# Kernel tuning notes

Measured on AMD Instinct MI355X. Metric: run time of the kernel, lower is better.

The kernel has to match this reference:

```python
import jax, jax.numpy as jnp
import numpy as np

silu = jax.nn.silu
B, L, H, IN = 128, 2048, 8, 37
NL = 8  # 4 encoder + 4 decoder SE3 layers, stacked


def _se3_layer(h, pos, eW1, eb1, eW2, eb2, pW1, pb1, pW2, nW1, nb1, nW2, nb2):
    # chain graph: row = 0..N-2, col = 1..N-1 (as in the torch arange edges)
    rel = pos[1:] - pos[:-1]                      # [N-1, 3]
    dist = jnp.linalg.norm(rel, axis=-1, keepdims=True)
    ef = jnp.concatenate([h[:-1], h[1:], dist], axis=-1)   # [N-1, 2H+1]
    ea = silu(ef @ eW1 + eb1) @ eW2 + eb2                   # edge_mlp
    dp = silu(ea @ pW1 + pb1) @ pW2                         # pos_mlp (no bias on last)
    pos_upd = jnp.zeros_like(pos).at[:-1].add(dp).at[1:].add(-dp)
    node_upd = jnp.zeros_like(h).at[:-1].add(ea).at[1:].add(ea)
    h_out = silu(jnp.concatenate([h, node_upd], axis=-1) @ nW1 + nb1) @ nW2 + nb2
    return h_out, pos + 0.1 * pos_upd


def setup_inputs() -> dict:
    key = jax.random.key(0)
    ks = jax.random.split(key, 64)
    i = iter(range(64))
    def p(shape, s=0.1):
        return (jax.random.normal(ks[next(i)], shape, jnp.float32) * s)
    inp = {
        "atom_positions": jax.random.normal(ks[next(i)], (B, L, IN, 3), jnp.float32),
        "atom_mask": (jax.random.uniform(ks[next(i)], (B, L, IN)) < 0.8).astype(jnp.float32),
        "emb_W": p((IN, H)), "emb_b": p((H,)),
        "posemb_W1": p((3, H)), "posemb_b1": p((H,)),
        "posemb_W2": p((H, H)), "posemb_b2": p((H,)),
        # stacked SE3 conv params: layers 0-3 encoder, 4-7 decoder
        "conv_eW1": p((NL, 2 * H + 1, H)), "conv_eb1": p((NL, H)),
        "conv_eW2": p((NL, H, H)), "conv_eb2": p((NL, H)),
        "conv_pW1": p((NL, H, H)), "conv_pb1": p((NL, H)),
        "conv_pW2": p((NL, H, 3)),
        "conv_nW1": p((NL, 2 * H, H)), "conv_nb1": p((NL, H)),
        "conv_nW2": p((NL, H, H)), "conv_nb2": p((NL, H)),
        "tol_W1": p((H, H)), "tol_b1": p((H,)),
        "tol_W2": p((H, H)), "tol_b2": p((H,)),
        "froml_W1": p((H, H)), "froml_b1": p((H,)),
        "froml_W2": p((H, H)), "froml_b2": p((H,)),
        "posdec_W1": p((H, 2 * H)), "posdec_b1": p((2 * H,)),
        "posdec_W2": p((2 * H, IN * 3)), "posdec_b2": p((IN * 3,)),
        "maskdec_W": p((H, IN)), "maskdec_b": p((IN,)),
    }
    return inp


def reference(atom_positions, atom_mask, emb_W, emb_b, posemb_W1, posemb_b1,
              posemb_W2, posemb_b2, conv_eW1, conv_eb1, conv_eW2, conv_eb2,
              conv_pW1, conv_pb1, conv_pW2, conv_nW1, conv_nb1, conv_nW2,
              conv_nb2, tol_W1, tol_b1, tol_W2, tol_b2, froml_W1, froml_b1,
              froml_W2, froml_b2, posdec_W1, posdec_b1, posdec_W2, posdec_b2,
              maskdec_W, maskdec_b):
    # ---- encode ----
    h = atom_mask @ emb_W + emb_b                              # [B,L,H]
    m = atom_mask[..., None]
    mean_pos = (atom_positions * m).sum(axis=2) / (m.sum(axis=2) + 1e-8)  # [B,L,3]
    pos_feat = silu(mean_pos @ posemb_W1 + posemb_b1) @ posemb_W2 + posemb_b2
    h = (h + pos_feat).reshape(B * L, H)
    pos = mean_pos.reshape(B * L, 3)
    for li in range(4):
        h, pos = _se3_layer(h, pos, conv_eW1[li], conv_eb1[li], conv_eW2[li],
                            conv_eb2[li], conv_pW1[li], conv_pb1[li], conv_pW2[li],
                            conv_nW1[li], conv_nb1[li], conv_nW2[li], conv_nb2[li])
    h = h.reshape(B, L, H)
    z = silu(h @ tol_W1 + tol_b1) @ tol_W2 + tol_b2            # [B,L,latent]
    # ---- decode ----
    h = silu(z @ froml_W1 + froml_b1) @ froml_W2 + froml_b2
    h = h.reshape(B * L, H)
    pos = pos  # already flat [B*L, 3]
    for li in range(4, 8):
        h, pos = _se3_layer(h, pos, conv_eW1[li], conv_eb1[li], conv_eW2[li],
                            conv_eb2[li], conv_pW1[li], conv_pb1[li], conv_pW2[li],
                            conv_nW1[li], conv_nb1[li], conv_nW2[li], conv_nb2[li])
    h = h.reshape(B, L, H)
    pos_out = (silu(h @ posdec_W1 + posdec_b1) @ posdec_W2 + posdec_b2)
    pos_out = pos_out.reshape(B, L, IN, 3)
    mask_out = h @ maskdec_W + maskdec_b                       # [B,L,IN]
    return pos_out, mask_out
```

## Files before the change

### kernel.cpp

```cpp
#include <hip/hip_runtime.h>

#define NTOT 262144
#define NLAY 8
#define TOUT 240

__device__ __forceinline__ float silu_f(float x) {
    return x * (1.0f / (1.0f + __expf(-x)));
}

__global__ __launch_bounds__(256) void k_encode(
    const float* __restrict__ ap, const float* __restrict__ amask,
    const float* __restrict__ embW, const float* __restrict__ embB,
    const float* __restrict__ peW1, const float* __restrict__ peB1,
    const float* __restrict__ peW2, const float* __restrict__ peB2,
    float* __restrict__ h0, float* __restrict__ pos0)
{
    __shared__ alignas(16) float sM[64 * 37];
    __shared__ alignas(16) float sA[64 * 111];
    __shared__ alignas(16) float sW[37 * 8];
    const int tid = threadIdx.x;
    const long nb = (long)blockIdx.x * 64;

    if (tid < 74) ((float4*)sW)[tid] = ((const float4*)embW)[tid];
    const float4* gm = (const float4*)(amask + nb * 37);
    float4* sm4 = (float4*)sM;
    #pragma unroll 1
    for (int i = tid; i < 64 * 37 / 4; i += 256) sm4[i] = gm[i];
    const float4* ga = (const float4*)(ap + nb * 111);
    float4* sa4 = (float4*)sA;
    #pragma unroll 1
    for (int i = tid; i < 64 * 111 / 4; i += 256) sa4[i] = ga[i];
    __syncthreads();

    const int n = tid >> 2;
    const int p = tid & 3;
    const int k0 = p * 10;
    const int k1 = (p == 3) ? 37 : k0 + 10;

    const float* mrow = sM + n * 37;
    const float* arow = sA + n * 111;
    float hacc[8] = {0, 0, 0, 0, 0, 0, 0, 0};
    float ps0 = 0.f, ps1 = 0.f, ps2 = 0.f, msum = 0.f;
    #pragma unroll 1
    for (int k = k0; k < k1; ++k) {
        float mv = mrow[k];
        msum += mv;
        const float4* wr = (const float4*)(sW + k * 8);
        float4 w0 = wr[0], w1 = wr[1];
        hacc[0] += mv * w0.x; hacc[1] += mv * w0.y;
        hacc[2] += mv * w0.z; hacc[3] += mv * w0.w;
        hacc[4] += mv * w1.x; hacc[5] += mv * w1.y;
        hacc[6] += mv * w1.z; hacc[7] += mv * w1.w;
        ps0 += mv * arow[k * 3 + 0];
        ps1 += mv * arow[k * 3 + 1];
        ps2 += mv * arow[k * 3 + 2];
    }
    #pragma unroll
    for (int m = 1; m <= 2; m <<= 1) {
        msum += __shfl_xor(msum, m);
        ps0 += __shfl_xor(ps0, m);
        ps1 += __shfl_xor(ps1, m);
        ps2 += __shfl_xor(ps2, m);
        #pragma unroll
        for (int j = 0; j < 8; ++j) hacc[j] += __shfl_xor(hacc[j], m);
    }

    float inv = 1.0f / (msum + 1e-8f);
    float mp0 = ps0 * inv, mp1 = ps1 * inv, mp2 = ps2 * inv;
    float q[8];
    #pragma unroll
    for (int j = 0; j < 8; ++j) {
        float a = peB1[j];
        a += mp0 * peW1[0 * 8 + j];
        a += mp1 * peW1[1 * 8 + j];
        a += mp2 * peW1[2 * 8 + j];
        q[j] = silu_f(a);
    }
    #pragma unroll
    for (int j = 0; j < 8; ++j) {
        float a = peB2[j] + embB[j];
        #pragma unroll
        for (int r = 0; r < 8; ++r) a += q[r] * peW2[r * 8 + j];
        hacc[j] += a;
    }
    const long g = nb + n;
    if (p == 0) ((float4*)(h0 + g * 8))[0] = make_float4(hacc[0], hacc[1], hacc[2], hacc[3]);
    if (p == 1) ((float4*)(h0 + g * 8))[1] = make_float4(hacc[4], hacc[5], hacc[6], hacc[7]);
    if (p == 2) ((float4*)pos0)[g] = make_float4(mp0, mp1, mp2, 0.f);
}

__global__ __launch_bounds__(256) void k_stack(
    const float* __restrict__ h0, const float* __restrict__ pos0,
    float* __restrict__ hfin,
    const float* __restrict__ ceW1, const float* __restrict__ ceB1,
    const float* __restrict__ ceW2, const float* __restrict__ ceB2,
    const float* __restrict__ cpW1, const float* __restrict__ cpB1,
    const float* __restrict__ cpW2,
    const float* __restrict__ cnW1, const float* __restrict__ cnB1,
    const float* __restrict__ cnW2, const float* __restrict__ cnB2,
    const float* __restrict__ tW1, const float* __restrict__ tB1,
    const float* __restrict__ tW2, const float* __restrict__ tB2,
    const float* __restrict__ fW1, const float* __restrict__ fB1,
    const float* __restrict__ fW2, const float* __restrict__ fB2)
{
    __shared__ float4 sH[512];
    __shared__ float4 sP[256];
    __shared__ float4 sE[512];
    __shared__ float4 sD[256];
    const int t = threadIdx.x;
    const int g0 = blockIdx.x * TOUT;
    const int g = g0 - 8 + t;

    float4 z4 = make_float4(0.f, 0.f, 0.f, 0.f);
    float4 ha = z4, hb = z4, pa = z4;
    if (g >= 0 && g < NTOT) {
        const float4* hp = (const float4*)(h0 + (long)g * 8);
        ha = hp[0];
        hb = hp[1];
        pa = ((const float4*)pos0)[g];
    }
    sH[t * 2] = ha;
    sH[t * 2 + 1] = hb;
    sP[t] = pa;
    __syncthreads();

    const int tp = (t < 255) ? (t + 1) : t;
    const int tm = (t > 0) ? (t - 1) : t;
    float hn[8] = {0, 0, 0, 0, 0, 0, 0, 0};

    #pragma unroll 1
    for (int li = 0; li < NLAY; ++li) {
        float hl[8], hr[8];
        {
            float4 a = sH[t * 2], b = sH[t * 2 + 1];
            hl[0] = a.x; hl[1] = a.y; hl[2] = a.z; hl[3] = a.w;
            hl[4] = b.x; hl[5] = b.y; hl[6] = b.z; hl[7] = b.w;
            float4 c = sH[tp * 2], d = sH[tp * 2 + 1];
            hr[0] = c.x; hr[1] = c.y; hr[2] = c.z; hr[3] = c.w;
            hr[4] = d.x; hr[5] = d.y; hr[6] = d.z; hr[7] = d.w;
        }
        float4 plv = sP[t], prv = sP[tp];
        float r0 = prv.x - plv.x, r1 = prv.y - plv.y, r2 = prv.z - plv.z;
        float dist = sqrtf(r0 * r0 + r1 * r1 + r2 * r2);

        const float* wE1 = ceW1 + li * 136;
        const float* bE1 = ceB1 + li * 8;
        const float* wE2 = ceW2 + li * 64;
        const float* bE2 = ceB2 + li * 8;
        const float* wP1 = cpW1 + li * 64;
        const float* bP1 = cpB1 + li * 8;
        const float* wP2 = cpW2 + li * 24;
        const float* wN1 = cnW1 + li * 128;
        const float* bN1 = cnB1 + li * 8;
        const float* wN2 = cnW2 + li * 64;
        const float* bN2 = cnB2 + li * 8;

        float t1[8];
        #pragma unroll
        for (int j = 0; j < 8; ++j) {
            float a = bE1[j];
            #pragma unroll
            for (int r = 0; r < 8; ++r) a += hl[r] * wE1[r * 8 + j];
            #pragma unroll
            for (int r = 0; r < 8; ++r) a += hr[r] * wE1[64 + r * 8 + j];
            a += dist * wE1[128 + j];
            t1[j] = silu_f(a);
        }
        float ea[8];
        #pragma unroll
        for (int j = 0; j < 8; ++j) {
            float a = bE2[j];
            #pragma unroll
            for (int r = 0; r < 8; ++r) a += t1[r] * wE2[r * 8 + j];
            ea[j] = a;
        }
        float q[8];
        #pragma unroll
        for (int j = 0; j < 8; ++j) {
            float a = bP1[j];
            #pragma unroll
            for (int r = 0; r < 8; ++r) a += ea[r] * wP1[r * 8 + j];
            q[j] = silu_f(a);
        }
        float dp0 = 0.f, dp1 = 0.f, dp2 = 0.f;
        #pragma unroll
        for (int r = 0; r < 8; ++r) {
            dp0 += q[r] * wP2[r * 3 + 0];
            dp1 += q[r] * wP2[r * 3 + 1];
            dp2 += q[r] * wP2[r * 3 + 2];
        }
        sE[t * 2] = make_float4(ea[0], ea[1], ea[2], ea[3]);
        sE[t * 2 + 1] = make_float4(ea[4], ea[5], ea[6], ea[7]);
        sD[t] = make_float4(dp0, dp1, dp2, 0.f);
        __syncthreads();

        float nu[8] = {0, 0, 0, 0, 0, 0, 0, 0};
        float pu0 = 0.f, pu1 = 0.f, pu2 = 0.f;
        if (g < NTOT - 1) {
            #pragma unroll
            for (int j = 0; j < 8; ++j) nu[j] += ea[j];
            pu0 += dp0; pu1 += dp1; pu2 += dp2;
        }
        if (g > 0) {
            float4 a = sE[tm * 2], b = sE[tm * 2 + 1];
            nu[0] += a.x; nu[1] += a.y; nu[2] += a.z; nu[3] += a.w;
            nu[4] += b.x; nu[5] += b.y; nu[6] += b.z; nu[7] += b.w;
            float4 dl = sD[tm];
            pu0 -= dl.x; pu1 -= dl.y; pu2 -= dl.z;
        }
        float u[8];
        #pragma unroll
        for (int j = 0; j < 8; ++j) {
            float a = bN1[j];
            #pragma unroll
            for (int r = 0; r < 8; ++r) a += hl[r] * wN1[r * 8 + j];
            #pragma unroll
            for (int r = 0; r < 8; ++r) a += nu[r] * wN1[64 + r * 8 + j];
            u[j] = silu_f(a);
        }
        #pragma unroll
        for (int j = 0; j < 8; ++j) {
            float a = bN2[j];
            #pragma unroll
            for (int r = 0; r < 8; ++r) a += u[r] * wN2[r * 8 + j];
            hn[j] = a;
        }
        float pn0 = plv.x + 0.1f * pu0;
        float pn1 = plv.y + 0.1f * pu1;
        float pn2 = plv.z + 0.1f * pu2;

        if (li == 3) {
            float a8[8];
            #pragma unroll
            for (int j = 0; j < 8; ++j) {
                float a = tB1[j];
                #pragma unroll
                for (int r = 0; r < 8; ++r) a += hn[r] * tW1[r * 8 + j];
                a8[j] = silu_f(a);
            }
            float zz[8];
            #pragma unroll
            for (int j = 0; j < 8; ++j) {
                float a = tB2[j];
                #pragma unroll
                for (int r = 0; r < 8; ++r) a += a8[r] * tW2[r * 8 + j];
                zz[j] = a;
            }
            float b8[8];
            #pragma unroll
            for (int j = 0; j < 8; ++j) {
                float a = fB1[j];
                #pragma unroll
                for (int r = 0; r < 8; ++r) a += zz[r] * fW1[r * 8 + j];
                b8[j] = silu_f(a);
            }
            #pragma unroll
            for (int j = 0; j < 8; ++j) {
                float a = fB2[j];
                #pragma unroll
                for (int r = 0; r < 8; ++r) a += b8[r] * fW2[r * 8 + j];
                hn[j] = a;
            }
        }

        const int winLo2 = max(0, g0 - 7 + li);
        const int winHi2 = min(NTOT, g0 + 247 - li);
        if (g >= winLo2 && g < winHi2) {
            sH[t * 2] = make_float4(hn[0], hn[1], hn[2], hn[3]);
            sH[t * 2 + 1] = make_float4(hn[4], hn[5], hn[6], hn[7]);
            sP[t] = make_float4(pn0, pn1, pn2, 0.f);
        }
        __syncthreads();
    }

    if (t >= 8 && t < 8 + TOUT && g < NTOT) {
        float4* hd = (float4*)(hfin + (long)g * 8);
        hd[0] = make_float4(hn[0], hn[1], hn[2], hn[3]);
        hd[1] = make_float4(hn[4], hn[5], hn[6], hn[7]);
    }
}

__global__ __launch_bounds__(256) void k_decode(
    const float* __restrict__ hfin,
    const float* __restrict__ dW1, const float* __restrict__ dB1,
    const float* __restrict__ dW2, const float* __restrict__ dB2,
    const float* __restrict__ mW, const float* __restrict__ mB,
    float* __restrict__ out)
{
    __shared__ alignas(16) float sh[128 * 8];
    __shared__ alignas(16) float st1[128 * 16];
    const int tid = threadIdx.x;
    const long nb = (long)blockIdx.x * 128;

    ((float4*)sh)[tid] = ((const float4*)(hfin + nb * 8))[tid];
    __syncthreads();

    {
        const int n = tid >> 1;
        const int c0 = (tid & 1) * 8;
        const float4* h4 = (const float4*)(sh + n * 8);
        float4 h0v = h4[0], h1v = h4[1];
        float hr[8] = {h0v.x, h0v.y, h0v.z, h0v.w, h1v.x, h1v.y, h1v.z, h1v.w};
        #pragma unroll
        for (int jj = 0; jj < 8; ++jj) {
            int j = c0 + jj;
            float a = dB1[j];
            #pragma unroll
            for (int r = 0; r < 8; ++r) a += hr[r] * dW1[r * 16 + j];
            st1[n * 16 + j] = silu_f(a);
        }
    }
    __syncthreads();

    if (tid < 222) {
        const int half = (tid >= 111) ? 1 : 0;
        const int j = tid - half * 111;
        float w[16];
        #pragma unroll
        for (int r = 0; r < 16; ++r) w[r] = dW2[r * 111 + j];
        const float bj = dB2[j];
        float* op = out + nb * 111 + j;
        #pragma unroll 2
        for (int n = half; n < 128; n += 2) {
            const float4* t4 = (const float4*)(st1 + n * 16);
            float4 a0 = t4[0], a1 = t4[1], a2 = t4[2], a3 = t4[3];
            float acc = bj;
            acc += a0.x * w[0] + a0.y * w[1] + a0.z * w[2] + a0.w * w[3];
            acc += a1.x * w[4] + a1.y * w[5] + a1.z * w[6] + a1.w * w[7];
            acc += a2.x * w[8] + a2.y * w[9] + a2.z * w[10] + a2.w * w[11];
            acc += a3.x * w[12] + a3.y * w[13] + a3.z * w[14] + a3.w * w[15];
            op[n * 111] = acc;
        }
        const int g6 = tid / 37;
        const int j2 = tid - g6 * 37;
        float wm[8];
        #pragma unroll
        for (int r = 0; r < 8; ++r) wm[r] = mW[r * 37 + j2];
        const float bm = mB[j2];
        float* omp_ = out + (long)NTOT * 111 + nb * 37 + j2;
        #pragma unroll 1
        for (int n = g6; n < 128; n += 6) {
            const float4* h4 = (const float4*)(sh + n * 8);
            float4 h0v = h4[0], h1v = h4[1];
            float acc = bm;
            acc += h0v.x * wm[0] + h0v.y * wm[1] + h0v.z * wm[2] + h0v.w * wm[3];
            acc += h1v.x * wm[4] + h1v.y * wm[5] + h1v.z * wm[6] + h1v.w * wm[7];
            omp_[n * 37] = acc;
        }
    }
}

extern "C" void kernel_launch(void* const* d_in, const int* in_sizes, int n_in,
                              void* d_out, int out_size, void* d_ws, size_t ws_size,
                              hipStream_t stream) {
    const float* ap     = (const float*)d_in[0];
    const float* amask  = (const float*)d_in[1];
    const float* embW   = (const float*)d_in[2];
    const float* embB   = (const float*)d_in[3];
    const float* peW1   = (const float*)d_in[4];
    const float* peB1   = (const float*)d_in[5];
    const float* peW2   = (const float*)d_in[6];
    const float* peB2   = (const float*)d_in[7];
    const float* ceW1   = (const float*)d_in[8];
    const float* ceB1   = (const float*)d_in[9];
    const float* ceW2   = (const float*)d_in[10];
    const float* ceB2   = (const float*)d_in[11];
    const float* cpW1   = (const float*)d_in[12];
    const float* cpB1   = (const float*)d_in[13];
    const float* cpW2   = (const float*)d_in[14];
    const float* cnW1   = (const float*)d_in[15];
    const float* cnB1   = (const float*)d_in[16];
    const float* cnW2   = (const float*)d_in[17];
    const float* cnB2   = (const float*)d_in[18];
    const float* tW1    = (const float*)d_in[19];
    const float* tB1    = (const float*)d_in[20];
    const float* tW2    = (const float*)d_in[21];
    const float* tB2    = (const float*)d_in[22];
    const float* fW1    = (const float*)d_in[23];
    const float* fB1    = (const float*)d_in[24];
    const float* fW2    = (const float*)d_in[25];
    const float* fB2    = (const float*)d_in[26];
    const float* dW1    = (const float*)d_in[27];
    const float* dB1    = (const float*)d_in[28];
    const float* dW2    = (const float*)d_in[29];
    const float* dB2    = (const float*)d_in[30];
    const float* mW     = (const float*)d_in[31];
    const float* mB     = (const float*)d_in[32];

    float* h0   = (float*)d_ws;
    float* pos0 = h0 + (size_t)NTOT * 8;
    float* hfin = pos0 + (size_t)NTOT * 4;
    float* out  = (float*)d_out;

    k_encode<<<NTOT / 64, 256, 0, stream>>>(ap, amask, embW, embB,
                                            peW1, peB1, peW2, peB2, h0, pos0);
    k_stack<<<(NTOT + TOUT - 1) / TOUT, 256, 0, stream>>>(
        h0, pos0, hfin,
        ceW1, ceB1, ceW2, ceB2, cpW1, cpB1, cpW2,
        cnW1, cnB1, cnW2, cnB2,
        tW1, tB1, tW2, tB2, fW1, fB1, fW2, fB2);
    k_decode<<<NTOT / 128, 256, 0, stream>>>(hfin, dW1, dB1, dW2, dB2, mW, mB, out);
}
```

Baseline: 435.0 us.

## Run SE3 layer stack per wavefront with shuffles instead of shared-memory barriers

The layer-stack kernel now assigns each 64-lane wavefront its own chain segment, with two nodes per lane. Neighbour features and edge messages are exchanged with lane shuffles instead of shared memory and block-wide barriers. This removes all LDS traffic and __syncthreads from the eight-layer loop. The cost is a larger relative halo (16 of 128 nodes recomputed versus 16 of 256). It also swaps divisions and sqrt for the hardware approximate rcp/sqrt builtins, which may change precision slightly.

```diff
diff --git a/kernel.cpp b/kernel.cpp
--- a/kernel.cpp
+++ b/kernel.cpp
@@ -2,10 +2,11 @@
 
 #define NTOT 262144
 #define NLAY 8
-#define TOUT 240
+#define SEGOUT 112
+#define NSEG ((NTOT + SEGOUT - 1) / SEGOUT)
 
 __device__ __forceinline__ float silu_f(float x) {
-    return x * (1.0f / (1.0f + __expf(-x)));
+    return x * __builtin_amdgcn_rcpf(1.0f + __expf(-x));
 }
 
 __global__ __launch_bounds__(256) void k_encode(
@@ -65,7 +66,7 @@
         for (int j = 0; j < 8; ++j) hacc[j] += __shfl_xor(hacc[j], m);
     }
 
-    float inv = 1.0f / (msum + 1e-8f);
+    float inv = __builtin_amdgcn_rcpf(msum + 1e-8f);
     float mp0 = ps0 * inv, mp1 = ps1 * inv, mp2 = ps2 * inv;
     float q[8];
     #pragma unroll
@@ -87,6 +88,115 @@
     if (p == 0) ((float4*)(h0 + g * 8))[0] = make_float4(hacc[0], hacc[1], hacc[2], hacc[3]);
     if (p == 1) ((float4*)(h0 + g * 8))[1] = make_float4(hacc[4], hacc[5], hacc[6], hacc[7]);
     if (p == 2) ((float4*)pos0)[g] = make_float4(mp0, mp1, mp2, 0.f);
+}
+
+
+__device__ __forceinline__ void edge_mlp(
+    const float* __restrict__ wE1, const float* __restrict__ bE1,
+    const float* __restrict__ wE2, const float* __restrict__ bE2,
+    const float* __restrict__ wP1, const float* __restrict__ bP1,
+    const float* __restrict__ wP2,
+    const float* hl, const float* hr, float r0, float r1, float r2,
+    float* ea, float& dp0, float& dp1, float& dp2)
+{
+    float dist = __builtin_amdgcn_sqrtf(r0 * r0 + r1 * r1 + r2 * r2);
+    float t1[8];
+    #pragma unroll
+    for (int j = 0; j < 8; ++j) {
+        float a = bE1[j];
+        #pragma unroll
+        for (int r = 0; r < 8; ++r) a += hl[r] * wE1[r * 8 + j];
+        #pragma unroll
+        for (int r = 0; r < 8; ++r) a += hr[r] * wE1[64 + r * 8 + j];
+        a += dist * wE1[128 + j];
+        t1[j] = silu_f(a);
+    }
+    #pragma unroll
+    for (int j = 0; j < 8; ++j) {
+        float a = bE2[j];
+        #pragma unroll
+        for (int r = 0; r < 8; ++r) a += t1[r] * wE2[r * 8 + j];
+        ea[j] = a;
+    }
+    float q[8];
+    #pragma unroll
+    for (int j = 0; j < 8; ++j) {
+        float a = bP1[j];
+        #pragma unroll
+        for (int r = 0; r < 8; ++r) a += ea[r] * wP1[r * 8 + j];
+        q[j] = silu_f(a);
+    }
+    dp0 = 0.f; dp1 = 0.f; dp2 = 0.f;
+    #pragma unroll
+    for (int r = 0; r < 8; ++r) {
+        dp0 += q[r] * wP2[r * 3 + 0];
+        dp1 += q[r] * wP2[r * 3 + 1];
+        dp2 += q[r] * wP2[r * 3 + 2];
+    }
+}
+
+__device__ __forceinline__ void node_mlp(
+    const float* __restrict__ wN1, const float* __restrict__ bN1,
+    const float* __restrict__ wN2, const float* __restrict__ bN2,
+    const float* hl, const float* nu, float* hn)
+{
+    float u[8];
+    #pragma unroll
+    for (int j = 0; j < 8; ++j) {
+        float a = bN1[j];
+        #pragma unroll
+        for (int r = 0; r < 8; ++r) a += hl[r] * wN1[r * 8 + j];
+        #pragma unroll
+        for (int r = 0; r < 8; ++r) a += nu[r] * wN1[64 + r * 8 + j];
+        u[j] = silu_f(a);
+    }
+    #pragma unroll
+    for (int j = 0; j < 8; ++j) {
+        float a = bN2[j];
+        #pragma unroll
+        for (int r = 0; r < 8; ++r) a += u[r] * wN2[r * 8 + j];
+        hn[j] = a;
+    }
+}
+
+__device__ __forceinline__ void latent_mlp(
+    const float* __restrict__ tW1, const float* __restrict__ tB1,
+    const float* __restrict__ tW2, const float* __restrict__ tB2,
+    const float* __restrict__ fW1, const float* __restrict__ fB1,
+    const float* __restrict__ fW2, const float* __restrict__ fB2,
+    float* hn)
+{
+    float a8[8];
+    #pragma unroll
+    for (int j = 0; j < 8; ++j) {
+        float a = tB1[j];
+        #pragma unroll
+        for (int r = 0; r < 8; ++r) a += hn[r] * tW1[r * 8 + j];
+        a8[j] = silu_f(a);
+    }
+    float zz[8];
+    #pragma unroll
+    for (int j = 0; j < 8; ++j) {
+        float a = tB2[j];
+        #pragma unroll
+        for (int r = 0; r < 8; ++r) a += a8[r] * tW2[r * 8 + j];
+        zz[j] = a;
+    }
+    float b8[8];
+    #pragma unroll
+    for (int j = 0; j < 8; ++j) {
+        float a = fB1[j];
+        #pragma unroll
+        for (int r = 0; r < 8; ++r) a += zz[r] * fW1[r * 8 + j];
+        b8[j] = silu_f(a);
+    }
+    #pragma unroll
+    for (int j = 0; j < 8; ++j) {
+        float a = fB2[j];
+        #pragma unroll
+        for (int r = 0; r < 8; ++r) a += b8[r] * fW2[r * 8 + j];
+        hn[j] = a;
+    }
 }
 
 __global__ __launch_bounds__(256) void k_stack(
@@ -103,46 +213,39 @@
     const float* __restrict__ fW1, const float* __restrict__ fB1,
     const float* __restrict__ fW2, const float* __restrict__ fB2)
 {
-    __shared__ float4 sH[512];
-    __shared__ float4 sP[256];
-    __shared__ float4 sE[512];
-    __shared__ float4 sD[256];
-    const int t = threadIdx.x;
-    const int g0 = blockIdx.x * TOUT;
-    const int g = g0 - 8 + t;
-
-    float4 z4 = make_float4(0.f, 0.f, 0.f, 0.f);
-    float4 ha = z4, hb = z4, pa = z4;
-    if (g >= 0 && g < NTOT) {
-        const float4* hp = (const float4*)(h0 + (long)g * 8);
-        ha = hp[0];
-        hb = hp[1];
-        pa = ((const float4*)pos0)[g];
-    }
-    sH[t * 2] = ha;
-    sH[t * 2 + 1] = hb;
-    sP[t] = pa;
-    __syncthreads();
-
-    const int tp = (t < 255) ? (t + 1) : t;
-    const int tm = (t > 0) ? (t - 1) : t;
-    float hn[8] = {0, 0, 0, 0, 0, 0, 0, 0};
+    const int lane = threadIdx.x & 63;
+    const int seg  = blockIdx.x * 4 + (threadIdx.x >> 6);
+    const int base = seg * SEGOUT - 8;
+    const int nA   = base + 2 * lane;
+    const int nB   = nA + 1;
+
+    float hA[8] = {0, 0, 0, 0, 0, 0, 0, 0};
+    float hB[8] = {0, 0, 0, 0, 0, 0, 0, 0};
+    float pA0 = 0.f, pA1 = 0.f, pA2 = 0.f;
+    float pB0 = 0.f, pB1 = 0.f, pB2 = 0.f;
+    if (nA >= 0 && nA < NTOT) {
+        const float4* hp = (const float4*)(h0 + (long)nA * 8);
+        float4 a = hp[0], b = hp[1];
+        hA[0] = a.x; hA[1] = a.y; hA[2] = a.z; hA[3] = a.w;
+        hA[4] = b.x; hA[5] = b.y; hA[6] = b.z; hA[7] = b.w;
+        float4 p = ((const float4*)pos0)[nA];
+        pA0 = p.x; pA1 = p.y; pA2 = p.z;
+    }
+    if (nB >= 0 && nB < NTOT) {
+        const float4* hp = (const float4*)(h0 + (long)nB * 8);
+        float4 a = hp[0], b = hp[1];
+        hB[0] = a.x; hB[1] = a.y; hB[2] = a.z; hB[3] = a.w;
+        hB[4] = b.x; hB[5] = b.y; hB[6] = b.z; hB[7] = b.w;
+        float4 p = ((const float4*)pos0)[nB];
+        pB0 = p.x; pB1 = p.y; pB2 = p.z;
+    }
+
+    const bool eA = (nA >= 0) && (nB < NTOT);
+    const bool eB = (nB >= 0) && (nB + 1 < NTOT);
+    const bool eL = (nA >= 1) && (nA < NTOT);
 
     #pragma unroll 1
     for (int li = 0; li < NLAY; ++li) {
-        float hl[8], hr[8];
-        {
-            float4 a = sH[t * 2], b = sH[t * 2 + 1];
-            hl[0] = a.x; hl[1] = a.y; hl[2] = a.z; hl[3] = a.w;
-            hl[4] = b.x; hl[5] = b.y; hl[6] = b.z; hl[7] = b.w;
-            float4 c = sH[tp * 2], d = sH[tp * 2 + 1];
-            hr[0] = c.x; hr[1] = c.y; hr[2] = c.z; hr[3] = c.w;
-            hr[4] = d.x; hr[5] = d.y; hr[6] = d.z; hr[7] = d.w;
-        }
-        float4 plv = sP[t], prv = sP[tp];
-        float r0 = prv.x - plv.x, r1 = prv.y - plv.y, r2 = prv.z - plv.z;
-        float dist = sqrtf(r0 * r0 + r1 * r1 + r2 * r2);
-
         const float* wE1 = ceW1 + li * 136;
         const float* bE1 = ceB1 + li * 8;
         const float* wE2 = ceW2 + li * 64;
@@ -155,128 +258,67 @@
         const float* wN2 = cnW2 + li * 64;
         const float* bN2 = cnB2 + li * 8;
 
-        float t1[8];
+        float hc[8], pc0, pc1, pc2;
+        #pragma unroll
+        for (int j = 0; j < 8; ++j) hc[j] = __shfl_down(hA[j], 1);
+        pc0 = __shfl_down(pA0, 1);
+        pc1 = __shfl_down(pA1, 1);
+        pc2 = __shfl_down(pA2, 1);
+
+        float eaA[8], dpA0, dpA1, dpA2;
+        edge_mlp(wE1, bE1, wE2, bE2, wP1, bP1, wP2,
+                 hA, hB, pB0 - pA0, pB1 - pA1, pB2 - pA2, eaA, dpA0, dpA1, dpA2);
+        float eaB[8], dpB0, dpB1, dpB2;
+        edge_mlp(wE1, bE1, wE2, bE2, wP1, bP1, wP2,
+                 hB, hc, pc0 - pB0, pc1 - pB1, pc2 - pB2, eaB, dpB0, dpB1, dpB2);
+
+        float eaL[8], dpL0, dpL1, dpL2;
+        #pragma unroll
+        for (int j = 0; j < 8; ++j) eaL[j] = __shfl_up(eaB[j], 1);
+        dpL0 = __shfl_up(dpB0, 1);
+        dpL1 = __shfl_up(dpB1, 1);
+        dpL2 = __shfl_up(dpB2, 1);
+
+        float nuA[8], nuB[8];
         #pragma unroll
         for (int j = 0; j < 8; ++j) {
-            float a = bE1[j];
-            #pragma unroll
-            for (int r = 0; r < 8; ++r) a += hl[r] * wE1[r * 8 + j];
-            #pragma unroll
-            for (int r = 0; r < 8; ++r) a += hr[r] * wE1[64 + r * 8 + j];
-            a += dist * wE1[128 + j];
-            t1[j] = silu_f(a);
-        }
-        float ea[8];
-        #pragma unroll
-        for (int j = 0; j < 8; ++j) {
-            float a = bE2[j];
-            #pragma unroll
-            for (int r = 0; r < 8; ++r) a += t1[r] * wE2[r * 8 + j];
-            ea[j] = a;
-        }
-        float q[8];
-        #pragma unroll
-        for (int j = 0; j < 8; ++j) {
-            float a = bP1[j];
-            #pragma unroll
-            for (int r = 0; r < 8; ++r) a += ea[r] * wP1[r * 8 + j];
-            q[j] = silu_f(a);
-        }
-        float dp0 = 0.f, dp1 = 0.f, dp2 = 0.f;
-        #pragma unroll
-        for (int r = 0; r < 8; ++r) {
-            dp0 += q[r] * wP2[r * 3 + 0];
-            dp1 += q[r] * wP2[r * 3 + 1];
-            dp2 += q[r] * wP2[r * 3 + 2];
-        }
-        sE[t * 2] = make_float4(ea[0], ea[1], ea[2], ea[3]);
-        sE[t * 2 + 1] = make_float4(ea[4], ea[5], ea[6], ea[7]);
-        sD[t] = make_float4(dp0, dp1, dp2, 0.f);
-        __syncthreads();
-
-        float nu[8] = {0, 0, 0, 0, 0, 0, 0, 0};
-        float pu0 = 0.f, pu1 = 0.f, pu2 = 0.f;
-        if (g < NTOT - 1) {
-            #pragma unroll
-            for (int j = 0; j < 8; ++j) nu[j] += ea[j];
-            pu0 += dp0; pu1 += dp1; pu2 += dp2;
-        }
-        if (g > 0) {
-            float4 a = sE[tm * 2], b = sE[tm * 2 + 1];
-            nu[0] += a.x; nu[1] += a.y; nu[2] += a.z; nu[3] += a.w;
-            nu[4] += b.x; nu[5] += b.y; nu[6] += b.z; nu[7] += b.w;
-            float4 dl = sD[tm];
-            pu0 -= dl.x; pu1 -= dl.y; pu2 -= dl.z;
-        }
-        float u[8];
-        #pragma unroll
-        for (int j = 0; j < 8; ++j) {
-            float a = bN1[j];
-            #pragma unroll
-            for (int r = 0; r < 8; ++r) a += hl[r] * wN1[r * 8 + j];
-            #pragma unroll
-            for (int r = 0; r < 8; ++r) a += nu[r] * wN1[64 + r * 8 + j];
-            u[j] = silu_f(a);
-        }
-        #pragma unroll
-        for (int j = 0; j < 8; ++j) {
-            float a = bN2[j];
-            #pragma unroll
-            for (int r = 0; r < 8; ++r) a += u[r] * wN2[r * 8 + j];
-            hn[j] = a;
-        }
-        float pn0 = plv.x + 0.1f * pu0;
-        float pn1 = plv.y + 0.1f * pu1;
-        float pn2 = plv.z + 0.1f * pu2;
+            nuA[j] = (eA ? eaA[j] : 0.f) + (eL ? eaL[j] : 0.f);
+            nuB[j] = (eB ? eaB[j] : 0.f) + (eA ? eaA[j] : 0.f);
+        }
+        float puA0 = (eA ? dpA0 : 0.f) - (eL ? dpL0 : 0.f);
+        float puA1 = (eA ? dpA1 : 0.f) - (eL ? dpL1 : 0.f);
+        float puA2 = (eA ? dpA2 : 0.f) - (eL ? dpL2 : 0.f);
+        float puB0 = (eB ? dpB0 : 0.f) - (eA ? dpA0 : 0.f);
+        float puB1 = (eB ? dpB1 : 0.f) - (eA ? dpA1 : 0.f);
+        float puB2 = (eB ? dpB2 : 0.f) - (eA ? dpA2 : 0.f);
+
+        float hnA[8], hnB[8];
+        node_mlp(wN1, bN1, wN2, bN2, hA, nuA, hnA);
+        node_mlp(wN1, bN1, wN2, bN2, hB, nuB, hnB);
+
+        pA0 += 0.1f * puA0; pA1 += 0.1f * puA1; pA2 += 0.1f * puA2;
+        pB0 += 0.1f * puB0; pB1 += 0.1f * puB1; pB2 += 0.1f * puB2;
 
         if (li == 3) {
-            float a8[8];
-            #pragma unroll
-            for (int j = 0; j < 8; ++j) {
-                float a = tB1[j];
-                #pragma unroll
-                for (int r = 0; r < 8; ++r) a += hn[r] * tW1[r * 8 + j];
-                a8[j] = silu_f(a);
-            }
-            float zz[8];
-            #pragma unroll
-            for (int j = 0; j < 8; ++j) {
-                float a = tB2[j];
-                #pragma unroll
-                for (int r = 0; r < 8; ++r) a += a8[r] * tW2[r * 8 + j];
-                zz[j] = a;
-            }
-            float b8[8];
-            #pragma unroll
-            for (int j = 0; j < 8; ++j) {
-                float a = fB1[j];
-                #pragma unroll
-                for (int r = 0; r < 8; ++r) a += zz[r] * fW1[r * 8 + j];
-                b8[j] = silu_f(a);
-            }
-            #pragma unroll
-            for (int j = 0; j < 8; ++j) {
-                float a = fB2[j];
-                #pragma unroll
-                for (int r = 0; r < 8; ++r) a += b8[r] * fW2[r * 8 + j];
-                hn[j] = a;
-            }
-        }
-
-        const int winLo2 = max(0, g0 - 7 + li);
-        const int winHi2 = min(NTOT, g0 + 247 - li);
-        if (g >= winLo2 && g < winHi2) {
-            sH[t * 2] = make_float4(hn[0], hn[1], hn[2], hn[3]);
-            sH[t * 2 + 1] = make_float4(hn[4], hn[5], hn[6], hn[7]);
-            sP[t] = make_float4(pn0, pn1, pn2, 0.f);
-        }
-        __syncthreads();
-    }
-
-    if (t >= 8 && t < 8 + TOUT && g < NTOT) {
-        float4* hd = (float4*)(hfin + (long)g * 8);
-        hd[0] = make_float4(hn[0], hn[1], hn[2], hn[3]);
-        hd[1] = make_float4(hn[4], hn[5], hn[6], hn[7]);
+            latent_mlp(tW1, tB1, tW2, tB2, fW1, fB1, fW2, fB2, hnA);
+            latent_mlp(tW1, tB1, tW2, tB2, fW1, fB1, fW2, fB2, hnB);
+        }
+
+        #pragma unroll
+        for (int j = 0; j < 8; ++j) { hA[j] = hnA[j]; hB[j] = hnB[j]; }
+    }
+
+    if (lane >= 4 && lane < 60) {
+        if (nA < NTOT) {
+            float4* hd = (float4*)(hfin + (long)nA * 8);
+            hd[0] = make_float4(hA[0], hA[1], hA[2], hA[3]);
+            hd[1] = make_float4(hA[4], hA[5], hA[6], hA[7]);
+        }
+        if (nB < NTOT) {
+            float4* hd = (float4*)(hfin + (long)nB * 8);
+            hd[0] = make_float4(hB[0], hB[1], hB[2], hB[3]);
+            hd[1] = make_float4(hB[4], hB[5], hB[6], hB[7]);
+        }
     }
 }
 
@@ -394,7 +436,8 @@
 
     k_encode<<<NTOT / 64, 256, 0, stream>>>(ap, amask, embW, embB,
                                             peW1, peB1, peW2, peB2, h0, pos0);
-    k_stack<<<(NTOT + TOUT - 1) / TOUT, 256, 0, stream>>>(
+    const int nblk = (NSEG + 3) / 4;
+    k_stack<<<nblk, 256, 0, stream>>>(
         h0, pos0, hfin,
         ceW1, ceB1, ceW2, ceB2, cpW1, cpB1, cpW2,
         cnW1, cnB1, cnW2, cnB2,
```

Measured after the change: 447.0 us. 2.8% more time.
